# Kernel optimization log

Measured on AMD Instinct MI355X. Metric: run time of the kernel, lower is better.

## Reference

```python
import jax, jax.numpy as jnp
import numpy as np

COMMITMENT_FACTOR = 0.25
QUANTIZATION_FACTOR = 1.0


def setup_inputs() -> dict:
    key = jax.random.key(0)
    k1, k2 = jax.random.split(key)
    B, D, H, W = 64, 256, 32, 32
    K = 1024
    z = jax.random.normal(k1, (B, D, H, W), dtype=jnp.float32)
    # torch init: uniform(-1/K, 1/K)
    codebook = jax.random.uniform(k2, (K, D), dtype=jnp.float32,
                                  minval=-1.0 / K, maxval=1.0 / K)
    return {"z": z, "codebook": codebook}


def reference(z, codebook):
    # z: [B, D, H, W]; codebook: [K, D]
    B, D, H, W = z.shape
    z_nhwc = jnp.transpose(z, (0, 2, 3, 1))          # [B, H, W, D]
    z_flat = z_nhwc.reshape(-1, D)                    # [N, D]
    # squared euclidean distances: ||z||^2 + ||w||^2 - 2 z.w
    dist = (jnp.sum(z_flat ** 2, axis=-1, keepdims=True)
            + jnp.sum(codebook ** 2, axis=-1)
            - 2.0 * z_flat @ codebook.T)              # [N, K]
    closest = jnp.argmin(dist, axis=-1)               # [N]
    quantized_indices = closest.reshape(B, H, W)
    # one-hot @ codebook == gather
    q_flat = codebook[closest]                        # [N, D]
    quantized = q_flat.reshape(B, H, W, D)

    commitment_loss = jnp.sum((jax.lax.stop_gradient(quantized) - z_nhwc) ** 2)
    embedding_loss = jnp.sum((quantized - jax.lax.stop_gradient(z_nhwc)) ** 2)
    loss = commitment_loss * COMMITMENT_FACTOR + embedding_loss * QUANTIZATION_FACTOR

    # straight-through estimator
    quantized_st = z_nhwc + jax.lax.stop_gradient(quantized - z_nhwc)
    quantized_st = jnp.transpose(quantized_st, (0, 3, 1, 2))  # [B, D, H, W]
    quantized_indices = quantized_indices[:, None, :, :]       # [B, 1, H, W]
    return quantized_st, quantized_indices, loss
```

## Files before the change

kernel.cpp:

```cpp
#include <hip/hip_runtime.h>


#define IDX_OFF  16777216
#define LOSS_OFF 16842752

typedef __bf16 bf16x8 __attribute__((ext_vector_type(8)));
typedef float  f32x4  __attribute__((ext_vector_type(4)));

__global__ __launch_bounds__(256) void vq_prep(const float* __restrict__ cb,
                                               __bf16* __restrict__ cbh,
                                               float* __restrict__ sc1) {
    const int t = threadIdx.x;
    const int r = blockIdx.x * 16 + (t >> 4);
    const int d0 = (t & 15) * 16;
    const float* src = cb + (size_t)r * 256 + d0;
    __bf16* dst = cbh + (size_t)r * 256 + d0;
    float s = 0.f;
    float4 f[4];
    #pragma unroll
    for (int p = 0; p < 4; p++) f[p] = *(const float4*)(src + p * 4);
    bf16x8 v0, v1;
    #pragma unroll
    for (int p = 0; p < 4; p++) {
        s = fmaf(f[p].x, f[p].x, s); s = fmaf(f[p].y, f[p].y, s);
        s = fmaf(f[p].z, f[p].z, s); s = fmaf(f[p].w, f[p].w, s);
    }
    v0[0]=(__bf16)f[0].x; v0[1]=(__bf16)f[0].y; v0[2]=(__bf16)f[0].z; v0[3]=(__bf16)f[0].w;
    v0[4]=(__bf16)f[1].x; v0[5]=(__bf16)f[1].y; v0[6]=(__bf16)f[1].z; v0[7]=(__bf16)f[1].w;
    v1[0]=(__bf16)f[2].x; v1[1]=(__bf16)f[2].y; v1[2]=(__bf16)f[2].z; v1[3]=(__bf16)f[2].w;
    v1[4]=(__bf16)f[3].x; v1[5]=(__bf16)f[3].y; v1[6]=(__bf16)f[3].z; v1[7]=(__bf16)f[3].w;
    *(bf16x8*)dst = v0;
    *(bf16x8*)(dst + 8) = v1;
    s += __shfl_xor(s, 1, 64);
    s += __shfl_xor(s, 2, 64);
    s += __shfl_xor(s, 4, 64);
    s += __shfl_xor(s, 8, 64);
    if ((t & 15) == 0) sc1[r] = s + 1.0f;
}

__global__ __launch_bounds__(256, 2) void vq_mfma(const float* __restrict__ z,
                                                  const __bf16* __restrict__ cbh,
                                                  const float* __restrict__ sc1,
                                                  float* __restrict__ out) {
    __shared__ __align__(16) __bf16 z_s[64 * 256];
    __shared__ float red_s[4];

    const int t    = threadIdx.x;
    const int lane = t & 63;
    const int w    = t >> 6;
    const int m16  = lane & 15;
    const int q4   = lane >> 4;
    const int wc   = w << 5;
    const int blk  = blockIdx.x;
    const int b    = blk >> 4;
    const int hw0  = (blk & 15) << 6;
    const int n0   = blk << 6;
    const int kt0  = (blk & 3) << 8;

    bf16x8 bb0[2], bb1[2];
    {
        const __bf16* bp = cbh + (size_t)(kt0 + wc + m16) * 256 + q4 * 8;
        bb0[0] = *(const bf16x8*)bp;
        bb0[1] = *(const bf16x8*)(bp + 4096);
        bb1[0] = *(const bf16x8*)(bp + 32);
        bb1[1] = *(const bf16x8*)(bp + 32 + 4096);
    }

    float lz = 0.f;
    {
        const int rg    = (t & 15) * 4;
        const int dbase = (t >> 4) * 16;
        const float* zp = z + (size_t)b * 262144 + hw0 + rg;
        #pragma unroll
        for (int batch = 0; batch < 2; batch++) {
            float4 f[8];
            #pragma unroll
            for (int j = 0; j < 8; j++)
                f[j] = *(const float4*)(zp + (size_t)(dbase + batch * 8 + j) * 1024);
            const float* fp = (const float*)f;
            #pragma unroll
            for (int r = 0; r < 4; r++) {
                bf16x8 v;
                #pragma unroll
                for (int j = 0; j < 8; j++) {
                    float x = fp[j * 4 + r];
                    lz = fmaf(x, x, lz);
                    v[j] = (__bf16)x;
                }
                const int row = rg + r;
                const int gs  = ((t >> 4) * 2 + batch) ^ (row & 7);
                *(bf16x8*)&z_s[row * 256 + gs * 8] = v;
            }
        }
    }
    __syncthreads();

    unsigned int best[16];
    #pragma unroll
    for (int i = 0; i < 16; i++) best[i] = 0xFFFFFFFFu;

    bf16x8 a0[4];
    {
        const int gs = q4 ^ (m16 & 7);
        #pragma unroll
        for (int i = 0; i < 4; i++)
            a0[i] = *(const bf16x8*)&z_s[(i * 16 + m16) * 256 + gs * 8];
    }

    #pragma unroll 1
    for (int it = 0; it < 8; it++) {
        const int kt  = (kt0 + (it << 7)) & 1023;
        const int ktn = (kt0 + (((it + 1) & 7) << 7)) & 1023;
        int   kcv[2];
        float sck[2];
        #pragma unroll
        for (int j = 0; j < 2; j++) {
            kcv[j] = kt + wc + j * 16 + m16;
            sck[j] = sc1[kcv[j]];
        }
        const __bf16* bc  = cbh + (size_t)(kt + wc + m16) * 256 + q4 * 8;
        const __bf16* bnx = cbh + (size_t)(ktn + wc + m16) * 256 + q4 * 8;

        f32x4 acc[4][2];
        #pragma unroll
        for (int i = 0; i < 4; i++)
            #pragma unroll
            for (int j = 0; j < 2; j++) acc[i][j] = (f32x4){0.f, 0.f, 0.f, 0.f};

        #pragma unroll
        for (int dcs = 0; dcs < 8; dcs++) {
            const int dc = dcs * 32;
            bf16x8 bn[2];
            const __bf16* bp = (dcs < 6) ? (bc + dc + 64) : (bnx + (dc - 192));
            bn[0] = *(const bf16x8*)bp;
            bn[1] = *(const bf16x8*)(bp + 4096);

            bf16x8 an[4];
            {
                const int gs = ((((dc + 32) & 255) >> 3) + q4) ^ (m16 & 7);
                #pragma unroll
                for (int i = 0; i < 4; i++)
                    an[i] = *(const bf16x8*)&z_s[(i * 16 + m16) * 256 + gs * 8];
            }

            #pragma unroll
            for (int i = 0; i < 4; i++)
                #pragma unroll
                for (int j = 0; j < 2; j++)
                    acc[i][j] = __builtin_amdgcn_mfma_f32_16x16x32_bf16(a0[i], bb0[j], acc[i][j], 0, 0, 0);

            #pragma unroll
            for (int i = 0; i < 4; i++) a0[i] = an[i];
            bb0[0] = bb1[0]; bb0[1] = bb1[1];
            bb1[0] = bn[0];  bb1[1] = bn[1];
        }

        #pragma unroll
        for (int j = 0; j < 2; j++) {
            #pragma unroll
            for (int i = 0; i < 4; i++)
                #pragma unroll
                for (int r = 0; r < 4; r++) {
                    float v3 = fmaf(-2.f, acc[i][j][r], sck[j]);
                    unsigned int key = (__float_as_uint(v3) & 0xFFFFFC00u) | (unsigned int)kcv[j];
                    int pos = i * 4 + r;
                    best[pos] = min(best[pos], key);
                }
        }
    }

    #pragma unroll
    for (int pos = 0; pos < 16; pos++) {
        unsigned int k = best[pos];
        #pragma unroll
        for (int off = 1; off < 16; off <<= 1)
            k = min(k, (unsigned int)__shfl_xor((int)k, off, 64));
        best[pos] = k;
    }
    __syncthreads();

    unsigned int* ks = (unsigned int*)z_s;
    if (m16 == 0) {
        #pragma unroll
        for (int pos = 0; pos < 16; pos++) {
            int i = pos >> 2, r = pos & 3;
            int row = i * 16 + q4 * 4 + r;
            ks[w * 64 + row] = best[pos];
        }
    }
    __syncthreads();
    if (t < 64) {
        unsigned int key = min(min(ks[t], ks[64 + t]), min(ks[128 + t], ks[192 + t]));
        int kf = (int)(key & 1023u);
        ks[256 + t] = (unsigned int)kf;
        out[IDX_OFF + n0 + t] = (float)kf;
        lz += __uint_as_float(key & 0xFFFFFC00u) - 1.0f;
    }
    {
        float s = lz;
        #pragma unroll
        for (int off = 1; off < 64; off <<= 1) s += __shfl_xor(s, off, 64);
        if (lane == 0) red_s[w] = s;
    }
    __syncthreads();
    if (t == 0)
        atomicAdd(out + LOSS_OFF, 1.25f * ((red_s[0] + red_s[1]) + (red_s[2] + red_s[3])));

    const int qrow = t >> 2;
    const int qoff = (t & 3) * 64;
    const int myk  = (int)ks[256 + qrow];
    __syncthreads();
    {
        const __bf16* qp = cbh + (size_t)myk * 256 + qoff;
        #pragma unroll
        for (int p = 0; p < 8; p++) {
            bf16x8 v = *(const bf16x8*)(qp + p * 8);
            int gs = ((qoff >> 3) + p) ^ (qrow & 7);
            *(bf16x8*)&z_s[qrow * 256 + gs * 8] = v;
        }
    }
    __syncthreads();
    {
        const int nl   = t & 63;
        const int dseg = t >> 6;
        float* op = out + (size_t)(b * 256 + dseg * 64) * 1024 + hw0 + nl;
        #pragma unroll
        for (int p = 0; p < 8; p++) {
            int gs = (dseg * 8 + p) ^ (nl & 7);
            bf16x8 v = *(const bf16x8*)&z_s[nl * 256 + gs * 8];
            #pragma unroll
            for (int j = 0; j < 8; j++)
                op[(size_t)(p * 8 + j) * 1024] = (float)v[j];
        }
    }
}

extern "C" void kernel_launch(void* const* d_in, const int* in_sizes, int n_in,
                              void* d_out, int out_size, void* d_ws, size_t ws_size,
                              hipStream_t stream) {
    const float* z  = (const float*)d_in[0];
    const float* cb = (const float*)d_in[1];
    float* out = (float*)d_out;

    float*  sc1 = (float*)d_ws;
    __bf16* cbh = (__bf16*)((char*)d_ws + 8192);

    hipMemsetAsync(out + LOSS_OFF, 0, sizeof(float), stream);
    vq_prep<<<64, 256, 0, stream>>>(cb, cbh, sc1);
    vq_mfma<<<1024, 256, 0, stream>>>(z, cbh, sc1, out);
}
```

Baseline: 181.2 us.

## Store codebook in MFMA fragment-major layout and simplify operand prefetch pipeline

The prep kernel now also writes a copy of the bf16 codebook permuted so that each 16-row by 32-column MFMA B fragment is a contiguous 1 KB block. The main kernel reads B operands from this copy, so each wave's fragment load is fully coalesced instead of strided across 16 rows. The prefetch depth for B drops from two steps to one, and the A operands are now read from shared memory right before each MFMA instead of being double-buffered in registers. This lowers register pressure but exposes LDS latency more directly, and it adds an extra workspace buffer plus extra writes in the prep kernel.

```diff
diff --git a/kernel.cpp b/kernel.cpp
--- a/kernel.cpp
+++ b/kernel.cpp
@@ -9,6 +9,7 @@
 
 __global__ __launch_bounds__(256) void vq_prep(const float* __restrict__ cb,
                                                __bf16* __restrict__ cbh,
+                                               __bf16* __restrict__ cbf,
                                                float* __restrict__ sc1) {
     const int t = threadIdx.x;
     const int r = blockIdx.x * 16 + (t >> 4);
@@ -31,6 +32,11 @@
     v1[4]=(__bf16)f[3].x; v1[5]=(__bf16)f[3].y; v1[6]=(__bf16)f[3].z; v1[7]=(__bf16)f[3].w;
     *(bf16x8*)dst = v0;
     *(bf16x8*)(dst + 8) = v1;
+    {
+        const int slot = ((r >> 4) * 8 + (d0 >> 5)) * 512 + ((r & 15) * 4 + ((d0 >> 3) & 3)) * 8;
+        *(bf16x8*)&cbf[slot]     = v0;
+        *(bf16x8*)&cbf[slot + 8] = v1;
+    }
     s += __shfl_xor(s, 1, 64);
     s += __shfl_xor(s, 2, 64);
     s += __shfl_xor(s, 4, 64);
@@ -40,6 +46,7 @@
 
 __global__ __launch_bounds__(256, 2) void vq_mfma(const float* __restrict__ z,
                                                   const __bf16* __restrict__ cbh,
+                                                  const __bf16* __restrict__ cbf,
                                                   const float* __restrict__ sc1,
                                                   float* __restrict__ out) {
     __shared__ __align__(16) __bf16 z_s[64 * 256];
@@ -51,19 +58,18 @@
     const int m16  = lane & 15;
     const int q4   = lane >> 4;
     const int wc   = w << 5;
+    const int lidx = m16 * 4 + q4;
     const int blk  = blockIdx.x;
     const int b    = blk >> 4;
     const int hw0  = (blk & 15) << 6;
     const int n0   = blk << 6;
     const int kt0  = (blk & 3) << 8;
 
-    bf16x8 bb0[2], bb1[2];
-    {
-        const __bf16* bp = cbh + (size_t)(kt0 + wc + m16) * 256 + q4 * 8;
-        bb0[0] = *(const bf16x8*)bp;
-        bb0[1] = *(const bf16x8*)(bp + 4096);
-        bb1[0] = *(const bf16x8*)(bp + 32);
-        bb1[1] = *(const bf16x8*)(bp + 32 + 4096);
+    bf16x8 bb[2];
+    {
+        const __bf16* bp = cbf + (size_t)((kt0 + wc) >> 4) * 4096 + lidx * 8;
+        bb[0] = *(const bf16x8*)bp;
+        bb[1] = *(const bf16x8*)(bp + 4096);
     }
 
     float lz = 0.f;
@@ -99,14 +105,6 @@
     #pragma unroll
     for (int i = 0; i < 16; i++) best[i] = 0xFFFFFFFFu;
 
-    bf16x8 a0[4];
-    {
-        const int gs = q4 ^ (m16 & 7);
-        #pragma unroll
-        for (int i = 0; i < 4; i++)
-            a0[i] = *(const bf16x8*)&z_s[(i * 16 + m16) * 256 + gs * 8];
-    }
-
     #pragma unroll 1
     for (int it = 0; it < 8; it++) {
         const int kt  = (kt0 + (it << 7)) & 1023;
@@ -118,8 +116,8 @@
             kcv[j] = kt + wc + j * 16 + m16;
             sck[j] = sc1[kcv[j]];
         }
-        const __bf16* bc  = cbh + (size_t)(kt + wc + m16) * 256 + q4 * 8;
-        const __bf16* bnx = cbh + (size_t)(ktn + wc + m16) * 256 + q4 * 8;
+        const __bf16* bt  = cbf + (size_t)((kt  + wc) >> 4) * 4096 + lidx * 8;
+        const __bf16* btn = cbf + (size_t)((ktn + wc) >> 4) * 4096 + lidx * 8;
 
         f32x4 acc[4][2];
         #pragma unroll
@@ -131,28 +129,20 @@
         for (int dcs = 0; dcs < 8; dcs++) {
             const int dc = dcs * 32;
             bf16x8 bn[2];
-            const __bf16* bp = (dcs < 6) ? (bc + dc + 64) : (bnx + (dc - 192));
+            const __bf16* bp = (dcs < 7) ? (bt + (dcs + 1) * 512) : btn;
             bn[0] = *(const bf16x8*)bp;
             bn[1] = *(const bf16x8*)(bp + 4096);
 
-            bf16x8 an[4];
-            {
-                const int gs = ((((dc + 32) & 255) >> 3) + q4) ^ (m16 & 7);
-                #pragma unroll
-                for (int i = 0; i < 4; i++)
-                    an[i] = *(const bf16x8*)&z_s[(i * 16 + m16) * 256 + gs * 8];
+            const int gs = ((dc >> 3) + q4) ^ (m16 & 7);
+            #pragma unroll
+            for (int i = 0; i < 4; i++) {
+                bf16x8 a = *(const bf16x8*)&z_s[(i * 16 + m16) * 256 + gs * 8];
+                acc[i][0] = __builtin_amdgcn_mfma_f32_16x16x32_bf16(a, bb[0], acc[i][0], 0, 0, 0);
+                acc[i][1] = __builtin_amdgcn_mfma_f32_16x16x32_bf16(a, bb[1], acc[i][1], 0, 0, 0);
             }
 
-            #pragma unroll
-            for (int i = 0; i < 4; i++)
-                #pragma unroll
-                for (int j = 0; j < 2; j++)
-                    acc[i][j] = __builtin_amdgcn_mfma_f32_16x16x32_bf16(a0[i], bb0[j], acc[i][j], 0, 0, 0);
-
-            #pragma unroll
-            for (int i = 0; i < 4; i++) a0[i] = an[i];
-            bb0[0] = bb1[0]; bb0[1] = bb1[1];
-            bb1[0] = bn[0];  bb1[1] = bn[1];
+            bb[0] = bn[0];
+            bb[1] = bn[1];
         }
 
         #pragma unroll
@@ -244,8 +234,9 @@
 
     float*  sc1 = (float*)d_ws;
     __bf16* cbh = (__bf16*)((char*)d_ws + 8192);
+    __bf16* cbf = (__bf16*)((char*)d_ws + 8192 + 524288);
 
     hipMemsetAsync(out + LOSS_OFF, 0, sizeof(float), stream);
-    vq_prep<<<64, 256, 0, stream>>>(cb, cbh, sc1);
-    vq_mfma<<<1024, 256, 0, stream>>>(z, cbh, sc1, out);
+    vq_prep<<<64, 256, 0, stream>>>(cb, cbh, cbf, sc1);
+    vq_mfma<<<1024, 256, 0, stream>>>(z, cbh, cbf, sc1, out);
 }
```

Result: faster. 163.3 us (-9.9%).
